# Optimization experiments

Measured on AMD Instinct MI355X. Metric: run time of the kernel, lower is better.

## Reference

```python
import jax, jax.numpy as jnp
import numpy as np

KS = 7  # neighborhood kernel size

def _wn(v, g):
    # weight-normalized 1x1-conv weight: v [out,in], g [out]
    n = jnp.sqrt(jnp.sum(v * v, axis=1, keepdims=True))
    return v * (g[:, None] / n)

def _ln(x, gamma, beta, eps=1e-6):
    mu = jnp.mean(x, axis=-1, keepdims=True)
    var = jnp.mean(jnp.square(x - mu), axis=-1, keepdims=True)
    return (x - mu) * jax.lax.rsqrt(var + eps) * gamma + beta

def _up_nearest(c, H, W):
    # integer-factor nearest upsample on channels-last [B,h,w,C]
    rh, rw = H // c.shape[1], W // c.shape[2]
    return jnp.repeat(jnp.repeat(c, rh, axis=1), rw, axis=2)

def _adaln(x, cond, gamma, beta, v, g):
    xn = _ln(x, gamma, beta)
    cu = _up_nearest(jax.nn.silu(cond), x.shape[1], x.shape[2])
    ab = cu @ _wn(v, g).T
    a, b = jnp.split(ab, 2, axis=-1)
    return xn * (1.0 + a) + b

def _gate(x, cond, v, g):
    cu = _up_nearest(jax.nn.silu(cond), x.shape[1], x.shape[2])
    return x * (cu @ _wn(v, g).T)

def _neigh_idx(n, k):
    # NATTEN-style clamped window starts: each query sees exactly k in-bounds neighbors
    starts = np.clip(np.arange(n) - k // 2, 0, n - k)
    return jnp.asarray(starts[:, None] + np.arange(k))  # [n,k]

def _natten2d(x, w_qkv, b_qkv, w_out, b_out, n_heads):
    B, H, W, C = x.shape
    hd = C // n_heads
    qkv = x @ w_qkv.T + b_qkv
    q, k, v = jnp.split(qkv, 3, axis=-1)
    q = q.reshape(B, H, W, n_heads, hd)
    k = k.reshape(B, H, W, n_heads, hd)
    v = v.reshape(B, H, W, n_heads, hd)
    ih = _neigh_idx(H, KS)
    iw = _neigh_idx(W, KS)
    def gather(t):
        t = t[:, ih]            # [B,H,KS,W,nh,hd]
        t = t[:, :, :, iw]      # [B,H,KS,W,KS,nh,hd]
        t = jnp.transpose(t, (0, 1, 3, 5, 2, 4, 6))  # [B,H,W,nh,KS,KS,hd]
        return t.reshape(B, H, W, n_heads, KS * KS, hd)
    kn, vn = gather(k), gather(v)
    scale = jnp.asarray(1.0 / np.sqrt(hd), x.dtype)
    logits = jnp.einsum('bhwnd,bhwnkd->bhwnk', q, kn) * scale
    attn = jax.nn.softmax(logits, axis=-1)
    out = jnp.einsum('bhwnk,bhwnkd->bhwnd', attn, vn).reshape(B, H, W, C)
    return out @ w_out.T + b_out

def _mlp(x, w1, b1, w2, b2):
    return jax.nn.gelu(x @ w1.T + b1) @ w2.T + b2

def setup_inputs():
    key = jax.random.key(0)
    B, H, W, D, CD, NH = 2, 48, 48, 384, 384, 6
    ks = jax.random.split(key, 10)
    s = 0.02
    return dict(
        x=jax.random.normal(ks[0], (B, H, W, D), jnp.float32),
        cond=jax.random.normal(ks[1], (B, 6, 6, CD), jnp.float32),
        ln1_g=jnp.ones((D,), jnp.float32), ln1_b=jnp.zeros((D,), jnp.float32),
        ada1_v=jax.random.normal(ks[2], (2 * D, CD), jnp.float32) * s,
        ada1_g=jnp.ones((2 * D,), jnp.float32),
        ln2_g=jnp.ones((D,), jnp.float32), ln2_b=jnp.zeros((D,), jnp.float32),
        ada2_v=jax.random.normal(ks[3], (2 * D, CD), jnp.float32) * s,
        ada2_g=jnp.ones((2 * D,), jnp.float32),
        gate1_v=jax.random.normal(ks[4], (D, CD), jnp.float32) * s,
        gate1_g=jnp.ones((D,), jnp.float32),
        gate2_v=jax.random.normal(ks[5], (D, CD), jnp.float32) * s,
        gate2_g=jnp.ones((D,), jnp.float32),
        w_qkv=jax.random.normal(ks[6], (3 * D, D), jnp.float32) * s,
        b_qkv=jnp.zeros((3 * D,), jnp.float32),
        w_out=jax.random.normal(ks[7], (D, D), jnp.float32) * s,
        b_out=jnp.zeros((D,), jnp.float32),
        w_mlp1=jax.random.normal(ks[8], (4 * D, D), jnp.float32) * s,
        b_mlp1=jnp.zeros((4 * D,), jnp.float32),
        w_mlp2=jax.random.normal(ks[9], (D, 4 * D), jnp.float32) * s,
        b_mlp2=jnp.zeros((D,), jnp.float32),
        n_heads=NH,
    )

def reference(x, cond, ln1_g, ln1_b, ada1_v, ada1_g, ln2_g, ln2_b, ada2_v, ada2_g,
              gate1_v, gate1_g, gate2_v, gate2_g, w_qkv, b_qkv, w_out, b_out,
              w_mlp1, b_mlp1, w_mlp2, b_mlp2, n_heads):
    h = _adaln(x, cond, ln1_g, ln1_b, ada1_v, ada1_g)
    h = _natten2d(h, w_qkv, b_qkv, w_out, b_out, n_heads)
    h = _gate(h, cond, gate1_v, gate1_g)
    x = x + h
    h = _adaln(x, cond, ln2_g, ln2_b, ada2_v, ada2_g)
    h = _mlp(h, w_mlp1, b_mlp1, w_mlp2, b_mlp2)
    h = _gate(h, cond, gate2_v, gate2_g)
    return x + h
```

## Files before the change

### kernel.cpp

```cpp
#include <hip/hip_runtime.h>
#include <hip/hip_bf16.h>
#include <math.h>

#define NPIX 4608
#define D 384
#define CD 384
#define C3 1152
#define DMLP 1536
#define NCELL 72

typedef unsigned short u16;
typedef __attribute__((ext_vector_type(8))) short bf16x8;
typedef __attribute__((ext_vector_type(4))) float f32x4;

#define OFF_MOD   0
#define OFF_BIG   663552
#define OFF_HHI   28975104
#define OFF_HLO   32514048
#define OFF_AHI   36052992
#define OFF_ALO   39591936
#define OFF_MHI   43130880
#define OFF_MLO   57286656
#define OFF_WHI   71442432
#define OFF_WLO   74981376
#define MOD_ADA1  0
#define MOD_ADA2  55296
#define MOD_GATE1 110592
#define MOD_GATE2 138240
#define WOFF_QKV  0
#define WOFF_OUT  442368
#define WOFF_M1   589824
#define WOFF_M2   1179648

#define GLOAD16(g, l) __builtin_amdgcn_global_load_lds( \
    (const __attribute__((address_space(1))) unsigned int*)(g), \
    (__attribute__((address_space(3))) unsigned int*)(l), 16, 0, 0)

__device__ __forceinline__ float wsum(float v) {
    #pragma unroll
    for (int o = 32; o > 0; o >>= 1) v += __shfl_xor(v, o);
    return v;
}
__device__ __forceinline__ void split_bf16(float x, u16& h, u16& l) {
    __hip_bfloat16 bh = __float2bfloat16(x);
    float fh = __bfloat162float(bh);
    __hip_bfloat16 bl = __float2bfloat16(x - fh);
    h = *(u16*)&bh; l = *(u16*)&bl;
}

__global__ __launch_bounds__(256) void mod_kernel(
    const float* __restrict__ cond,
    const float* __restrict__ a1v, const float* __restrict__ a1g,
    const float* __restrict__ a2v, const float* __restrict__ a2g,
    const float* __restrict__ g1v, const float* __restrict__ g1g,
    const float* __restrict__ g2v, const float* __restrict__ g2g,
    float* __restrict__ mod)
{
    int wid  = (blockIdx.x * blockDim.x + threadIdx.x) >> 6;
    int lane = threadIdx.x & 63;
    int cell = wid / 2304;
    int row  = wid % 2304;

    const float* V; float g; float* dst; int r;
    if (row < 768)        { r = row;        V = a1v; g = a1g[r]; dst = mod + MOD_ADA1  + cell * 768 + r; }
    else if (row < 1536)  { r = row - 768;  V = a2v; g = a2g[r]; dst = mod + MOD_ADA2  + cell * 768 + r; }
    else if (row < 1920)  { r = row - 1536; V = g1v; g = g1g[r]; dst = mod + MOD_GATE1 + cell * 384 + r; }
    else                  { r = row - 1920; V = g2v; g = g2g[r]; dst = mod + MOD_GATE2 + cell * 384 + r; }

    const float* vrow = V + r * CD;
    const float* crow = cond + cell * CD;
    float dot = 0.f, nrm = 0.f;
    #pragma unroll
    for (int j = 0; j < 6; j++) {
        int k = lane + 64 * j;
        float c  = crow[k];
        float sc = c / (1.f + __expf(-c));
        float v  = vrow[k];
        dot += sc * v;
        nrm += v * v;
    }
    dot = wsum(dot);
    nrm = wsum(nrm);
    if (lane == 0) *dst = dot * g / sqrtf(nrm);
}

__global__ __launch_bounds__(256) void wconv_kernel(
    const float* __restrict__ wq, const float* __restrict__ wo,
    const float* __restrict__ w1, const float* __restrict__ w2,
    u16* __restrict__ whi, u16* __restrict__ wlo)
{
    int i4 = blockIdx.x * 256 + threadIdx.x;
    const float* src; int l4;
    if (i4 < 110592)        { src = wq; l4 = i4; }
    else if (i4 < 147456)   { src = wo; l4 = i4 - 110592; }
    else if (i4 < 294912)   { src = w1; l4 = i4 - 147456; }
    else                    { src = w2; l4 = i4 - 294912; }
    float4 v = ((const float4*)src)[l4];
    int o = i4 * 4;
    split_bf16(v.x, whi[o+0], wlo[o+0]);
    split_bf16(v.y, whi[o+1], wlo[o+1]);
    split_bf16(v.z, whi[o+2], wlo[o+2]);
    split_bf16(v.w, whi[o+3], wlo[o+3]);
}

__global__ __launch_bounds__(256) void adaln_kernel(
    const float* __restrict__ x,
    const float* __restrict__ gamma, const float* __restrict__ beta,
    const float* __restrict__ mod_ab,
    u16* __restrict__ ohi, u16* __restrict__ olo)
{
    int p    = (blockIdx.x * blockDim.x + threadIdx.x) >> 6;
    int lane = threadIdx.x & 63;
    int b  = p / 2304;
    int hh = (p / 48) % 48;
    int ww = p % 48;
    int cell = b * 36 + (hh >> 3) * 6 + (ww >> 3);

    const float* xr = x + (size_t)p * D;
    float v[6]; float s = 0.f, ss = 0.f;
    #pragma unroll
    for (int j = 0; j < 6; j++) {
        v[j] = xr[lane + 64 * j];
        s  += v[j];
        ss += v[j] * v[j];
    }
    s = wsum(s); ss = wsum(ss);
    float mu  = s * (1.f / 384.f);
    float var = ss * (1.f / 384.f) - mu * mu;
    float rs  = 1.f / sqrtf(var + 1e-6f);

    const float* ab = mod_ab + cell * 768;
    #pragma unroll
    for (int j = 0; j < 6; j++) {
        int d = lane + 64 * j;
        float xn = (v[j] - mu) * rs * gamma[d] + beta[d];
        float o  = xn * (1.f + ab[d]) + ab[384 + d];
        split_bf16(o, ohi[(size_t)p * D + d], olo[(size_t)p * D + d]);
    }
}

template <int EPI, int NS>
__global__ __launch_bounds__(256) void gemm_mfma(
    const u16* __restrict__ Ah, const u16* __restrict__ Al,
    const u16* __restrict__ Bh, const u16* __restrict__ Bl,
    const float* __restrict__ bias,
    float* __restrict__ Cf, u16* __restrict__ Ch, u16* __restrict__ Cl,
    int N, int K)
{
    __shared__ u16 lds[24576];
    const int tid  = threadIdx.x;
    const int lane = tid & 63;
    const int wid  = tid >> 6;

    const int nwg = gridDim.x;
    const int q = nwg >> 3, r = nwg & 7;
    const int xcd = blockIdx.x & 7, loc = blockIdx.x >> 3;
    const int wgid = (xcd < r ? xcd * (q + 1) : r * (q + 1) + (xcd - r) * q) + loc;

    const int nx = N >> 6;
    const int per = nx * 36;
    const int bz  = wgid / per;
    const int id2 = wgid - bz * per;
    const int by  = id2 / nx;
    const int bx  = id2 - by * nx;

    const int m0 = by * 128;
    const int n0 = bx * 64;
    const int kPer = K / NS;
    const int kbeg = bz * kPer;
    const int nt = kPer >> 5;

    const int wr = wid >> 1, wc = wid & 1;

    const u16* gsrc[6];
    int loff[6];
    #pragma unroll
    for (int s = 0; s < 6; s++) {
        int c = tid + (s << 8);
        const u16* base; int ks, row;
        if (c < 512)        { ks = c >> 7;           row = c & 127; base = Ah + (size_t)(m0 + row) * K; }
        else if (c < 1024)  { int cc = c - 512;  ks = cc >> 7; row = cc & 127; base = Al + (size_t)(m0 + row) * K; }
        else if (c < 1280)  { int cc = c - 1024; ks = cc >> 6; row = cc & 63;  base = Bh + (size_t)(n0 + row) * K; }
        else                { int cc = c - 1280; ks = cc >> 6; row = cc & 63;  base = Bl + (size_t)(n0 + row) * K; }
        gsrc[s] = base + ks * 8;
        loff[s] = c * 8;
    }

    f32x4 acc[4][2] = {};
    const int ks = lane >> 4;
    const int fr = lane & 15;

    #pragma unroll
    for (int s = 0; s < 6; s++) GLOAD16(gsrc[s] + kbeg, &lds[loff[s]]);
    __syncthreads();

    int cur = 0;
    for (int kt = 0; kt < nt; kt++) {
        if (kt + 1 < nt) {
            int k0 = kbeg + ((kt + 1) << 5);
            int dbo = (cur ^ 1) * 12288;
            #pragma unroll
            for (int s = 0; s < 6; s++) GLOAD16(gsrc[s] + k0, &lds[dbo + loff[s]]);
        }
        const int b0 = cur * 12288;
        bf16x8 ah[4], al[4], bh[2], bl[2];
        #pragma unroll
        for (int m = 0; m < 4; m++) {
            int ai = b0 + (ks * 128 + wr * 64 + m * 16 + fr) * 8;
            ah[m] = *(const bf16x8*)&lds[ai];
            al[m] = *(const bf16x8*)&lds[4096 + ai];
        }
        #pragma unroll
        for (int n = 0; n < 2; n++) {
            int bi = b0 + (ks * 64 + wc * 32 + n * 16 + fr) * 8;
            bh[n] = *(const bf16x8*)&lds[8192 + bi];
            bl[n] = *(const bf16x8*)&lds[10240 + bi];
        }
        #pragma unroll
        for (int m = 0; m < 4; m++)
            #pragma unroll
            for (int n = 0; n < 2; n++) {
                acc[m][n] = __builtin_amdgcn_mfma_f32_16x16x32_bf16(ah[m], bh[n], acc[m][n], 0, 0, 0);
                acc[m][n] = __builtin_amdgcn_mfma_f32_16x16x32_bf16(ah[m], bl[n], acc[m][n], 0, 0, 0);
                acc[m][n] = __builtin_amdgcn_mfma_f32_16x16x32_bf16(al[m], bh[n], acc[m][n], 0, 0, 0);
            }
        __syncthreads();
        cur ^= 1;
    }

    const int r4 = ks * 4;
    #pragma unroll
    for (int m = 0; m < 4; m++) {
        #pragma unroll
        for (int n = 0; n < 2; n++) {
            #pragma unroll
            for (int j = 0; j < 4; j++) {
                int row = m0 + wr * 64 + m * 16 + r4 + j;
                int col = n0 + wc * 32 + n * 16 + fr;
                float v = acc[m][n][j];
                if (EPI == 0) {
                    Cf[(size_t)row * N + col] = v + bias[col];
                } else if (EPI == 1) {
                    float t = v + bias[col];
                    float c = 0.7978845608028654f * (t + 0.044715f * t * t * t);
                    float e = __expf(2.f * c);
                    float th = (e - 1.f) / (e + 1.f);
                    float g = 0.5f * t * (1.f + th);
                    size_t idx = (size_t)row * N + col;
                    split_bf16(g, Ch[idx], Cl[idx]);
                } else {
                    Cf[((size_t)bz * NPIX + row) * N + col] = v;
                }
            }
        }
    }
}

__global__ __launch_bounds__(256) void reduce_gate(
    const float* __restrict__ part, const float* __restrict__ bias,
    const float* __restrict__ gate, const float* __restrict__ resid,
    float* __restrict__ out)
{
    int i4 = blockIdx.x * 256 + threadIdx.x;
    int row = i4 / 96, c4 = i4 % 96;
    int b  = row / 2304;
    int hh = (row / 48) % 48;
    int ww = row % 48;
    int cell = b * 36 + (hh >> 3) * 6 + (ww >> 3);

    const float4* P = (const float4*)part;
    float4 p0 = P[i4], p1 = P[i4 + 442368], p2 = P[i4 + 2 * 442368], p3 = P[i4 + 3 * 442368];
    float4 bb = ((const float4*)bias)[c4];
    float4 gg = ((const float4*)(gate + cell * 384))[c4];
    float4 rr = ((const float4*)resid)[i4];
    float4 o;
    o.x = rr.x + (p0.x + p1.x + p2.x + p3.x + bb.x) * gg.x;
    o.y = rr.y + (p0.y + p1.y + p2.y + p3.y + bb.y) * gg.y;
    o.z = rr.z + (p0.z + p1.z + p2.z + p3.z + bb.z) * gg.z;
    o.w = rr.w + (p0.w + p1.w + p2.w + p3.w + bb.w) * gg.w;
    ((float4*)out)[i4] = o;
}

__global__ __launch_bounds__(256) void natten_kernel(
    const float* __restrict__ qkv, u16* __restrict__ ohi, u16* __restrict__ olo)
{
    int wid  = (blockIdx.x * blockDim.x + threadIdx.x) >> 6;
    int lane = threadIdx.x & 63;
    int head = wid % 6;
    int p    = wid / 6;
    int b  = p / 2304;
    int hh = (p / 48) % 48;
    int ww = p % 48;
    int sh = hh - 3; sh = sh < 0 ? 0 : (sh > 41 ? 41 : sh);
    int sw = ww - 3; sw = sw < 0 ? 0 : (sw > 41 ? 41 : sw);
    int pb = b * 2304;

    const int n_sub = lane >> 3;
    const int d_sub = lane & 7;
    const int dof = head * 64 + d_sub * 8;

    const float* qp = qkv + (size_t)p * C3 + dof;
    float4 q0 = *(const float4*)qp;
    float4 q1 = *(const float4*)(qp + 4);
    q0.x *= 0.125f; q0.y *= 0.125f; q0.z *= 0.125f; q0.w *= 0.125f;
    q1.x *= 0.125f; q1.y *= 0.125f; q1.z *= 0.125f; q1.w *= 0.125f;

    float L[7];
    #pragma unroll
    for (int t = 0; t < 7; t++) {
        int n = t * 8 + n_sub;
        int nn = n > 48 ? 48 : n;
        int nr = nn / 7, nc = nn - nr * 7;
        const float* kp = qkv + (size_t)(pb + (sh + nr) * 48 + (sw + nc)) * C3 + 384 + dof;
        float4 k0 = *(const float4*)kp;
        float4 k1 = *(const float4*)(kp + 4);
        float d = q0.x * k0.x + q0.y * k0.y + q0.z * k0.z + q0.w * k0.w
                + q1.x * k1.x + q1.y * k1.y + q1.z * k1.z + q1.w * k1.w;
        d += __shfl_xor(d, 1);
        d += __shfl_xor(d, 2);
        d += __shfl_xor(d, 4);
        L[t] = (n < 49) ? d : -INFINITY;
    }

    float m = L[0];
    #pragma unroll
    for (int t = 1; t < 7; t++) m = fmaxf(m, L[t]);
    m = fmaxf(m, __shfl_xor(m, 8));
    m = fmaxf(m, __shfl_xor(m, 16));
    m = fmaxf(m, __shfl_xor(m, 32));

    float w[7]; float s = 0.f;
    #pragma unroll
    for (int t = 0; t < 7; t++) {
        w[t] = (L[t] == -INFINITY) ? 0.f : __expf(L[t] - m);
        s += w[t];
    }
    s += __shfl_xor(s, 8);
    s += __shfl_xor(s, 16);
    s += __shfl_xor(s, 32);
    float inv = 1.f / s;
    #pragma unroll
    for (int t = 0; t < 7; t++) w[t] *= inv;

    float a0x = 0.f, a0y = 0.f, a0z = 0.f, a0w = 0.f;
    float a1x = 0.f, a1y = 0.f, a1z = 0.f, a1w = 0.f;
    #pragma unroll
    for (int t = 0; t < 7; t++) {
        int n = t * 8 + n_sub;
        int nn = n > 48 ? 48 : n;
        int nr = nn / 7, nc = nn - nr * 7;
        const float* vp = qkv + (size_t)(pb + (sh + nr) * 48 + (sw + nc)) * C3 + 768 + dof;
        float4 v0 = *(const float4*)vp;
        float4 v1 = *(const float4*)(vp + 4);
        float wn = w[t];
        a0x = fmaf(wn, v0.x, a0x); a0y = fmaf(wn, v0.y, a0y);
        a0z = fmaf(wn, v0.z, a0z); a0w = fmaf(wn, v0.w, a0w);
        a1x = fmaf(wn, v1.x, a1x); a1y = fmaf(wn, v1.y, a1y);
        a1z = fmaf(wn, v1.z, a1z); a1w = fmaf(wn, v1.w, a1w);
    }
    #pragma unroll
    for (int o = 8; o <= 32; o <<= 1) {
        a0x += __shfl_xor(a0x, o); a0y += __shfl_xor(a0y, o);
        a0z += __shfl_xor(a0z, o); a0w += __shfl_xor(a0w, o);
        a1x += __shfl_xor(a1x, o); a1y += __shfl_xor(a1y, o);
        a1z += __shfl_xor(a1z, o); a1w += __shfl_xor(a1w, o);
    }

    if (lane < 8) {
        float av[8] = {a0x, a0y, a0z, a0w, a1x, a1y, a1z, a1w};
        u16 hi8[8], lo8[8];
        #pragma unroll
        for (int i = 0; i < 8; i++) split_bf16(av[i], hi8[i], lo8[i]);
        size_t oi = (size_t)p * D + head * 64 + lane * 8;
        *(uint4*)(ohi + oi) = *(uint4*)hi8;
        *(uint4*)(olo + oi) = *(uint4*)lo8;
    }
}

extern "C" void kernel_launch(void* const* d_in, const int* in_sizes, int n_in,
                              void* d_out, int out_size, void* d_ws, size_t ws_size,
                              hipStream_t stream)
{
    (void)in_sizes; (void)n_in; (void)out_size; (void)ws_size;
    const float* x      = (const float*)d_in[0];
    const float* cond   = (const float*)d_in[1];
    const float* ln1_g  = (const float*)d_in[2];
    const float* ln1_b  = (const float*)d_in[3];
    const float* ada1_v = (const float*)d_in[4];
    const float* ada1_g = (const float*)d_in[5];
    const float* ln2_g  = (const float*)d_in[6];
    const float* ln2_b  = (const float*)d_in[7];
    const float* ada2_v = (const float*)d_in[8];
    const float* ada2_g = (const float*)d_in[9];
    const float* gate1_v = (const float*)d_in[10];
    const float* gate1_g = (const float*)d_in[11];
    const float* gate2_v = (const float*)d_in[12];
    const float* gate2_g = (const float*)d_in[13];
    const float* w_qkv  = (const float*)d_in[14];
    const float* b_qkv  = (const float*)d_in[15];
    const float* w_out  = (const float*)d_in[16];
    const float* b_out  = (const float*)d_in[17];
    const float* w_mlp1 = (const float*)d_in[18];
    const float* b_mlp1 = (const float*)d_in[19];
    const float* w_mlp2 = (const float*)d_in[20];
    const float* b_mlp2 = (const float*)d_in[21];

    char* ws = (char*)d_ws;
    float* mod  = (float*)(ws + OFF_MOD);
    float* big  = (float*)(ws + OFF_BIG);
    u16* h_hi   = (u16*)(ws + OFF_HHI);
    u16* h_lo   = (u16*)(ws + OFF_HLO);
    u16* a_hi   = (u16*)(ws + OFF_AHI);
    u16* a_lo   = (u16*)(ws + OFF_ALO);
    u16* m_hi   = (u16*)(ws + OFF_MHI);
    u16* m_lo   = (u16*)(ws + OFF_MLO);
    u16* w_hi   = (u16*)(ws + OFF_WHI);
    u16* w_lo   = (u16*)(ws + OFF_WLO);
    float* x2   = (float*)d_out;

    mod_kernel<<<(NCELL * 2304) / 4, 256, 0, stream>>>(
        cond, ada1_v, ada1_g, ada2_v, ada2_g, gate1_v, gate1_g, gate2_v, gate2_g, mod);

    wconv_kernel<<<1728, 256, 0, stream>>>(w_qkv, w_out, w_mlp1, w_mlp2, w_hi, w_lo);

    adaln_kernel<<<NPIX / 4, 256, 0, stream>>>(x, ln1_g, ln1_b, mod + MOD_ADA1, h_hi, h_lo);

    gemm_mfma<0, 1><<<648, 256, 0, stream>>>(
        h_hi, h_lo, w_hi + WOFF_QKV, w_lo + WOFF_QKV, b_qkv,
        big, nullptr, nullptr, C3, D);

    natten_kernel<<<(NPIX * 6) / 4, 256, 0, stream>>>(big, a_hi, a_lo);

    gemm_mfma<2, 4><<<864, 256, 0, stream>>>(
        a_hi, a_lo, w_hi + WOFF_OUT, w_lo + WOFF_OUT, nullptr,
        big, nullptr, nullptr, D, D);

    reduce_gate<<<1728, 256, 0, stream>>>(big, b_out, mod + MOD_GATE1, x, x2);

    adaln_kernel<<<NPIX / 4, 256, 0, stream>>>(x2, ln2_g, ln2_b, mod + MOD_ADA2, h_hi, h_lo);

    gemm_mfma<1, 1><<<864, 256, 0, stream>>>(
        h_hi, h_lo, w_hi + WOFF_M1, w_lo + WOFF_M1, b_mlp1,
        nullptr, m_hi, m_lo, DMLP, D);

    gemm_mfma<2, 4><<<864, 256, 0, stream>>>(
        m_hi, m_lo, w_hi + WOFF_M2, w_lo + WOFF_M2, nullptr,
        big, nullptr, nullptr, D, DMLP);

    reduce_gate<<<1728, 256, 0, stream>>>(big, b_mlp2, mod + MOD_GATE2, x2, x2);
}
```

Baseline: 358.3 us.

## Compute AdaLN/gate modulation as an MFMA GEMM with factored weight norm

Replaces the per-(cell,row) dot-product kernel with a precompute of per-row weight-norm scales and bf16 hi/lo split silu(cond), followed by a split-bf16 MFMA GEMM over all modulation weights. The modulation tensor is re-laid out as [cell][2304], and the consumers' offsets and strides are updated. This removes the redundant reloading of the modulation weights for every cell and the repeated norm computation, at the cost of an extra launch and bf16-split precision.

```diff
diff --git a/kernel.cpp b/kernel.cpp
--- a/kernel.cpp
+++ b/kernel.cpp
@@ -23,10 +23,11 @@
 #define OFF_MLO   57286656
 #define OFF_WHI   71442432
 #define OFF_WLO   74981376
-#define MOD_ADA1  0
-#define MOD_ADA2  55296
-#define MOD_GATE1 110592
-#define MOD_GATE2 138240
+#define BIGOFF_MODV_HI  0
+#define BIGOFF_MODV_LO  1769472
+#define BIGOFF_SC_HI    3538944
+#define BIGOFF_SC_LO    3637248
+#define BIGOFF_INVN     3735552
 #define WOFF_QKV  0
 #define WOFF_OUT  442368
 #define WOFF_M1   589824
@@ -48,59 +49,160 @@
     h = *(u16*)&bh; l = *(u16*)&bl;
 }
 
-__global__ __launch_bounds__(256) void mod_kernel(
+__global__ __launch_bounds__(256) void wconv_kernel(
+    const float* __restrict__ wq, const float* __restrict__ wo,
+    const float* __restrict__ w1, const float* __restrict__ w2,
+    const float* __restrict__ a1v, const float* __restrict__ a2v,
+    const float* __restrict__ g1v, const float* __restrict__ g2v,
+    u16* __restrict__ whi, u16* __restrict__ wlo,
+    u16* __restrict__ mvhi, u16* __restrict__ mvlo)
+{
+    int i4 = blockIdx.x * 256 + threadIdx.x;
+    const float* src; int l4; u16 *dh, *dl; int o;
+    if (i4 < 442368) {
+        if (i4 < 110592)        { src = wq; l4 = i4; }
+        else if (i4 < 147456)   { src = wo; l4 = i4 - 110592; }
+        else if (i4 < 294912)   { src = w1; l4 = i4 - 147456; }
+        else                    { src = w2; l4 = i4 - 294912; }
+        dh = whi; dl = wlo; o = i4 * 4;
+    } else {
+        int j4 = i4 - 442368;
+        if (j4 < 73728)         { src = a1v; l4 = j4; }
+        else if (j4 < 147456)   { src = a2v; l4 = j4 - 73728; }
+        else if (j4 < 184320)   { src = g1v; l4 = j4 - 147456; }
+        else                    { src = g2v; l4 = j4 - 184320; }
+        dh = mvhi; dl = mvlo; o = j4 * 4;
+    }
+    float4 v = ((const float4*)src)[l4];
+    split_bf16(v.x, dh[o+0], dl[o+0]);
+    split_bf16(v.y, dh[o+1], dl[o+1]);
+    split_bf16(v.z, dh[o+2], dl[o+2]);
+    split_bf16(v.w, dh[o+3], dl[o+3]);
+}
+
+__global__ __launch_bounds__(256) void modprep_kernel(
     const float* __restrict__ cond,
     const float* __restrict__ a1v, const float* __restrict__ a1g,
     const float* __restrict__ a2v, const float* __restrict__ a2g,
     const float* __restrict__ g1v, const float* __restrict__ g1g,
     const float* __restrict__ g2v, const float* __restrict__ g2g,
-    float* __restrict__ mod)
+    float* __restrict__ invn, u16* __restrict__ schi, u16* __restrict__ sclo)
 {
     int wid  = (blockIdx.x * blockDim.x + threadIdx.x) >> 6;
     int lane = threadIdx.x & 63;
-    int cell = wid / 2304;
-    int row  = wid % 2304;
-
-    const float* V; float g; float* dst; int r;
-    if (row < 768)        { r = row;        V = a1v; g = a1g[r]; dst = mod + MOD_ADA1  + cell * 768 + r; }
-    else if (row < 1536)  { r = row - 768;  V = a2v; g = a2g[r]; dst = mod + MOD_ADA2  + cell * 768 + r; }
-    else if (row < 1920)  { r = row - 1536; V = g1v; g = g1g[r]; dst = mod + MOD_GATE1 + cell * 384 + r; }
-    else                  { r = row - 1920; V = g2v; g = g2g[r]; dst = mod + MOD_GATE2 + cell * 384 + r; }
-
-    const float* vrow = V + r * CD;
-    const float* crow = cond + cell * CD;
-    float dot = 0.f, nrm = 0.f;
-    #pragma unroll
-    for (int j = 0; j < 6; j++) {
-        int k = lane + 64 * j;
-        float c  = crow[k];
-        float sc = c / (1.f + __expf(-c));
-        float v  = vrow[k];
-        dot += sc * v;
-        nrm += v * v;
-    }
-    dot = wsum(dot);
-    nrm = wsum(nrm);
-    if (lane == 0) *dst = dot * g / sqrtf(nrm);
-}
-
-__global__ __launch_bounds__(256) void wconv_kernel(
-    const float* __restrict__ wq, const float* __restrict__ wo,
-    const float* __restrict__ w1, const float* __restrict__ w2,
-    u16* __restrict__ whi, u16* __restrict__ wlo)
-{
-    int i4 = blockIdx.x * 256 + threadIdx.x;
-    const float* src; int l4;
-    if (i4 < 110592)        { src = wq; l4 = i4; }
-    else if (i4 < 147456)   { src = wo; l4 = i4 - 110592; }
-    else if (i4 < 294912)   { src = w1; l4 = i4 - 147456; }
-    else                    { src = w2; l4 = i4 - 294912; }
-    float4 v = ((const float4*)src)[l4];
-    int o = i4 * 4;
-    split_bf16(v.x, whi[o+0], wlo[o+0]);
-    split_bf16(v.y, whi[o+1], wlo[o+1]);
-    split_bf16(v.z, whi[o+2], wlo[o+2]);
-    split_bf16(v.w, whi[o+3], wlo[o+3]);
+    if (wid < 2304) {
+        const float* V; float g; int r;
+        if (wid < 768)        { r = wid;        V = a1v; g = a1g[r]; }
+        else if (wid < 1536)  { r = wid - 768;  V = a2v; g = a2g[r]; }
+        else if (wid < 1920)  { r = wid - 1536; V = g1v; g = g1g[r]; }
+        else                  { r = wid - 1920; V = g2v; g = g2g[r]; }
+        const float* vrow = V + r * CD;
+        float nrm = 0.f;
+        #pragma unroll
+        for (int j = 0; j < 6; j++) {
+            float v = vrow[lane + 64 * j];
+            nrm += v * v;
+        }
+        nrm = wsum(nrm);
+        if (lane == 0) invn[wid] = g / sqrtf(nrm);
+    } else {
+        int cell = wid - 2304;
+        #pragma unroll
+        for (int j = 0; j < 6; j++) {
+            int k = lane + 64 * j;
+            float val = 0.f;
+            if (cell < NCELL) {
+                float c = cond[cell * CD + k];
+                val = c / (1.f + __expf(-c));
+            }
+            split_bf16(val, schi[cell * CD + k], sclo[cell * CD + k]);
+        }
+    }
+}
+
+__global__ __launch_bounds__(256) void modgemm_mfma(
+    const u16* __restrict__ Ah, const u16* __restrict__ Al,
+    const u16* __restrict__ Bh, const u16* __restrict__ Bl,
+    const float* __restrict__ invn, float* __restrict__ mod)
+{
+    __shared__ u16 lds[24576];
+    const int tid  = threadIdx.x;
+    const int lane = tid & 63;
+    const int wid  = tid >> 6;
+    const int n0 = blockIdx.x * 64;
+    const int K = 384, nt = 12;
+    const int wr = wid >> 1, wc = wid & 1;
+
+    const u16* gsrc[6];
+    int loff[6];
+    #pragma unroll
+    for (int s = 0; s < 6; s++) {
+        int c = tid + (s << 8);
+        const u16* base; int ks, row;
+        if (c < 512)        { ks = c >> 7;           row = c & 127; base = Ah + (size_t)row * K; }
+        else if (c < 1024)  { int cc = c - 512;  ks = cc >> 7; row = cc & 127; base = Al + (size_t)row * K; }
+        else if (c < 1280)  { int cc = c - 1024; ks = cc >> 6; row = cc & 63;  base = Bh + (size_t)(n0 + row) * K; }
+        else                { int cc = c - 1280; ks = cc >> 6; row = cc & 63;  base = Bl + (size_t)(n0 + row) * K; }
+        gsrc[s] = base + ks * 8;
+        loff[s] = c * 8;
+    }
+
+    f32x4 acc[4][2] = {};
+    const int ks = lane >> 4;
+    const int fr = lane & 15;
+
+    #pragma unroll
+    for (int s = 0; s < 6; s++) GLOAD16(gsrc[s], &lds[loff[s]]);
+    __syncthreads();
+
+    int cur = 0;
+    for (int kt = 0; kt < nt; kt++) {
+        if (kt + 1 < nt) {
+            int k0 = (kt + 1) << 5;
+            int dbo = (cur ^ 1) * 12288;
+            #pragma unroll
+            for (int s = 0; s < 6; s++) GLOAD16(gsrc[s] + k0, &lds[dbo + loff[s]]);
+        }
+        const int b0 = cur * 12288;
+        bf16x8 ah[4], al[4], bh[2], bl[2];
+        #pragma unroll
+        for (int m = 0; m < 4; m++) {
+            int ai = b0 + (ks * 128 + wr * 64 + m * 16 + fr) * 8;
+            ah[m] = *(const bf16x8*)&lds[ai];
+            al[m] = *(const bf16x8*)&lds[4096 + ai];
+        }
+        #pragma unroll
+        for (int n = 0; n < 2; n++) {
+            int bi = b0 + (ks * 64 + wc * 32 + n * 16 + fr) * 8;
+            bh[n] = *(const bf16x8*)&lds[8192 + bi];
+            bl[n] = *(const bf16x8*)&lds[10240 + bi];
+        }
+        #pragma unroll
+        for (int m = 0; m < 4; m++)
+            #pragma unroll
+            for (int n = 0; n < 2; n++) {
+                acc[m][n] = __builtin_amdgcn_mfma_f32_16x16x32_bf16(ah[m], bh[n], acc[m][n], 0, 0, 0);
+                acc[m][n] = __builtin_amdgcn_mfma_f32_16x16x32_bf16(ah[m], bl[n], acc[m][n], 0, 0, 0);
+                acc[m][n] = __builtin_amdgcn_mfma_f32_16x16x32_bf16(al[m], bh[n], acc[m][n], 0, 0, 0);
+            }
+        __syncthreads();
+        cur ^= 1;
+    }
+
+    const int r4 = ks * 4;
+    #pragma unroll
+    for (int m = 0; m < 4; m++) {
+        #pragma unroll
+        for (int n = 0; n < 2; n++) {
+            #pragma unroll
+            for (int j = 0; j < 4; j++) {
+                int row = wr * 64 + m * 16 + r4 + j;
+                int col = n0 + wc * 32 + n * 16 + fr;
+                if (row < NCELL)
+                    mod[(size_t)row * 2304 + col] = acc[m][n][j] * invn[col];
+            }
+        }
+    }
 }
 
 __global__ __launch_bounds__(256) void adaln_kernel(
@@ -129,7 +231,7 @@
     float var = ss * (1.f / 384.f) - mu * mu;
     float rs  = 1.f / sqrtf(var + 1e-6f);
 
-    const float* ab = mod_ab + cell * 768;
+    const float* ab = mod_ab + (size_t)cell * 2304;
     #pragma unroll
     for (int j = 0; j < 6; j++) {
         int d = lane + 64 * j;
@@ -271,7 +373,7 @@
     const float4* P = (const float4*)part;
     float4 p0 = P[i4], p1 = P[i4 + 442368], p2 = P[i4 + 2 * 442368], p3 = P[i4 + 3 * 442368];
     float4 bb = ((const float4*)bias)[c4];
-    float4 gg = ((const float4*)(gate + cell * 384))[c4];
+    float4 gg = ((const float4*)(gate + (size_t)cell * 2304))[c4];
     float4 rr = ((const float4*)resid)[i4];
     float4 o;
     o.x = rr.x + (p0.x + p1.x + p2.x + p3.x + bb.x) * gg.x;
@@ -416,14 +518,25 @@
     u16* m_lo   = (u16*)(ws + OFF_MLO);
     u16* w_hi   = (u16*)(ws + OFF_WHI);
     u16* w_lo   = (u16*)(ws + OFF_WLO);
+    char* bigc  = ws + OFF_BIG;
+    u16* mv_hi  = (u16*)(bigc + BIGOFF_MODV_HI);
+    u16* mv_lo  = (u16*)(bigc + BIGOFF_MODV_LO);
+    u16* sc_hi  = (u16*)(bigc + BIGOFF_SC_HI);
+    u16* sc_lo  = (u16*)(bigc + BIGOFF_SC_LO);
+    float* invn = (float*)(bigc + BIGOFF_INVN);
     float* x2   = (float*)d_out;
 
-    mod_kernel<<<(NCELL * 2304) / 4, 256, 0, stream>>>(
-        cond, ada1_v, ada1_g, ada2_v, ada2_g, gate1_v, gate1_g, gate2_v, gate2_g, mod);
-
-    wconv_kernel<<<1728, 256, 0, stream>>>(w_qkv, w_out, w_mlp1, w_mlp2, w_hi, w_lo);
-
-    adaln_kernel<<<NPIX / 4, 256, 0, stream>>>(x, ln1_g, ln1_b, mod + MOD_ADA1, h_hi, h_lo);
+    wconv_kernel<<<2592, 256, 0, stream>>>(
+        w_qkv, w_out, w_mlp1, w_mlp2, ada1_v, ada2_v, gate1_v, gate2_v,
+        w_hi, w_lo, mv_hi, mv_lo);
+
+    modprep_kernel<<<608, 256, 0, stream>>>(
+        cond, ada1_v, ada1_g, ada2_v, ada2_g, gate1_v, gate1_g, gate2_v, gate2_g,
+        invn, sc_hi, sc_lo);
+
+    modgemm_mfma<<<36, 256, 0, stream>>>(sc_hi, sc_lo, mv_hi, mv_lo, invn, mod);
+
+    adaln_kernel<<<NPIX / 4, 256, 0, stream>>>(x, ln1_g, ln1_b, mod, h_hi, h_lo);
 
     gemm_mfma<0, 1><<<648, 256, 0, stream>>>(
         h_hi, h_lo, w_hi + WOFF_QKV, w_lo + WOFF_QKV, b_qkv,
@@ -435,9 +548,9 @@
         a_hi, a_lo, w_hi + WOFF_OUT, w_lo + WOFF_OUT, nullptr,
         big, nullptr, nullptr, D, D);
 
-    reduce_gate<<<1728, 256, 0, stream>>>(big, b_out, mod + MOD_GATE1, x, x2);
-
-    adaln_kernel<<<NPIX / 4, 256, 0, stream>>>(x2, ln2_g, ln2_b, mod + MOD_ADA2, h_hi, h_lo);
+    reduce_gate<<<1728, 256, 0, stream>>>(big, b_out, mod + 1536, x, x2);
+
+    adaln_kernel<<<NPIX / 4, 256, 0, stream>>>(x2, ln2_g, ln2_b, mod + 768, h_hi, h_lo);
 
     gemm_mfma<1, 1><<<864, 256, 0, stream>>>(
         h_hi, h_lo, w_hi + WOFF_M1, w_lo + WOFF_M1, b_mlp1,
@@ -447,5 +560,5 @@
         m_hi, m_lo, w_hi + WOFF_M2, w_lo + WOFF_M2, nullptr,
         big, nullptr, nullptr, D, DMLP);
 
-    reduce_gate<<<1728, 256, 0, stream>>>(big, b_mlp2, mod + MOD_GATE2, x2, x2);
-}
+    reduce_gate<<<1728, 256, 0, stream>>>(big, b_mlp2, mod + 1920, x2, x2);
+}
```

Result: faster. 331.8 us (-7.4%).
